# Kernel optimization log

Hardware: AMD Instinct MI355X
Metric: run time of the kernel (lower is better)

## Reference

```python
import jax, jax.numpy as jnp
import numpy as np

B, S, D = 2, 2048, 1024
H, HD = 16, 64
WIN = 256


def setup_inputs() -> dict:
    key = jax.random.key(0)
    ks = jax.random.split(key, 9)
    scale = 0.02
    x = jax.random.normal(ks[0], (B, S, D), dtype=jnp.float32)
    Wq = jax.random.normal(ks[1], (D, H * HD), dtype=jnp.float32) * scale
    Wk = jax.random.normal(ks[2], (D, H * HD), dtype=jnp.float32) * scale
    Wv = jax.random.normal(ks[3], (D, H * HD), dtype=jnp.float32) * scale
    Wo = jax.random.normal(ks[4], (H * HD, D), dtype=jnp.float32) * scale
    bq = jnp.zeros((H * HD,), jnp.float32)
    bk = jnp.zeros((H * HD,), jnp.float32)
    bv = jnp.zeros((H * HD,), jnp.float32)
    bo = jnp.zeros((D,), jnp.float32)
    return {"x": x, "Wq": Wq, "bq": bq, "Wk": Wk, "bk": bk,
            "Wv": Wv, "bv": bv, "Wo": Wo, "bo": bo}


def _band_mask(seq_len, window):
    # True where attention is DISALLOWED (matches torch masked positions).
    # mask=None in the original => prefix_size=0, row i attends to
    # j in [max(0, i - window), i]  (causal sliding window).
    i = jnp.arange(seq_len)[:, None]
    j = jnp.arange(seq_len)[None, :]
    return (j > i) | (j < i - window)


def reference(x, Wq, bq, Wk, bk, Wv, bv, Wo, bo):
    b, s, _ = x.shape
    q = (x @ Wq + bq).reshape(b, s, H, HD)
    k = (x @ Wk + bk).reshape(b, s, H, HD)
    v = (x @ Wv + bv).reshape(b, s, H, HD)
    scores = jnp.einsum("bihd,bjhd->bhij", q, k) / jnp.sqrt(jnp.float32(HD))
    mask = _band_mask(s, WIN)  # [s, s], broadcasts over batch, heads
    scores = jnp.where(mask[None, None, :, :], -jnp.inf, scores)
    attn = jax.nn.softmax(scores, axis=-1)  # dropout is identity at eval
    out = jnp.einsum("bhij,bjhd->bihd", attn, v).reshape(b, s, H * HD)
    return out @ Wo + bo
```

## Files before the change

kernel.cpp:

```cpp
#include <hip/hip_runtime.h>
#include <stdint.h>
#include <stddef.h>

#define S_LEN 2048
#define DMODEL 1024
#define NHEAD 16
#define HDIM 64
#define WINSZ 256
#define MROWS 4096
#define NQKV 3072

typedef __bf16 bf16x8 __attribute__((ext_vector_type(8)));
typedef float f32x4 __attribute__((ext_vector_type(4)));
typedef unsigned short us4 __attribute__((ext_vector_type(4)));
typedef unsigned short us8 __attribute__((ext_vector_type(8)));

#define MFMA16(a, b, c) __builtin_amdgcn_mfma_f32_16x16x32_bf16((a), (b), (c), 0, 0, 0)

__device__ __forceinline__ unsigned short f2b(float f) {
  union { float f; unsigned u; } v; v.f = f;
  unsigned u = v.u;
  unsigned r = (u + 0x7FFFu + ((u >> 16) & 1u)) >> 16;
  return (unsigned short)r;
}
__device__ __forceinline__ void storev(float* p, float v) { *p = v; }
__device__ __forceinline__ void storev(unsigned short* p, float v) { *p = f2b(v); }

__device__ __forceinline__ void gload_lds16(const unsigned short* g, unsigned short* l) {
  __builtin_amdgcn_global_load_lds(
      (const __attribute__((address_space(1))) unsigned int*)g,
      (__attribute__((address_space(3))) unsigned int*)l, 16, 0, 0);
}


__global__ void prep_kernel(const float* __restrict__ x,
                            const float* __restrict__ Wq, const float* __restrict__ Wk,
                            const float* __restrict__ Wv, const float* __restrict__ Wo,
                            const float* __restrict__ bq, const float* __restrict__ bk,
                            const float* __restrict__ bv,
                            unsigned short* __restrict__ xb, unsigned short* __restrict__ WqkvT,
                            unsigned short* __restrict__ WoT, float* __restrict__ bqkv) {
  __shared__ float tile[32][33];
  const int bid = blockIdx.x;
  const int tid = threadIdx.x;
  if (bid < 4096) {
    int i = (bid * 256 + tid) * 4;
    float4 v = *reinterpret_cast<const float4*>(x + i);
    us4 o;
    o[0] = f2b(v.x); o[1] = f2b(v.y); o[2] = f2b(v.z); o[3] = f2b(v.w);
    *reinterpret_cast<us4*>(xb + i) = o;
  } else if (bid < 8192) {
    int z = (bid - 4096) >> 10;
    int rem = (bid - 4096) & 1023;
    int bx = rem & 31, by = rem >> 5;
    const float* W = (z == 0) ? Wq : (z == 1) ? Wk : (z == 2) ? Wv : Wo;
    unsigned short* Wt = (z == 3) ? WoT : WqkvT + (size_t)z * DMODEL * DMODEL;
    int n0 = bx * 32, k0 = by * 32;
    int tx = tid & 31, ty = tid >> 5;
#pragma unroll
    for (int i = 0; i < 32; i += 8)
      tile[ty + i][tx] = W[(size_t)(k0 + ty + i) * DMODEL + n0 + tx];
    __syncthreads();
#pragma unroll
    for (int i = 0; i < 32; i += 8)
      Wt[(size_t)(n0 + ty + i) * DMODEL + k0 + tx] = f2b(tile[tx][ty + i]);
  } else {
    int i = (bid - 8192) * 256 + tid;
    if (i < DMODEL) {
      bqkv[i] = bq[i];
      bqkv[DMODEL + i] = bk[i];
      bqkv[2 * DMODEL + i] = bv[i];
    }
  }
}


__global__ __launch_bounds__(512, 4) void gemm8p_kernel(
    const unsigned short* __restrict__ A, const unsigned short* __restrict__ Bt,
    const float* __restrict__ bias, unsigned short* __restrict__ C, int N, int K) {
  __shared__ unsigned short As[2 * 128 * 64];
  __shared__ unsigned short Bs[2 * 192 * 64];
  const int tid = threadIdx.x;
  const int cpx = gridDim.x >> 3;
  const int nid = (blockIdx.x & 7) * cpx + (blockIdx.x >> 3);
  const int nbx = N / 192;
  const int by = nid / nbx, bx = nid - by * nbx;
  const int m0 = by * 128, n0 = bx * 192;
  const int wid = tid >> 6, l = tid & 63;
  const int wm = wid >> 2, wn = wid & 3;
  const int lr = l & 15, lg = l >> 4;
  const int srow = tid >> 3;
  const int scol = (tid & 7) * 8;
  const int scol_g = scol ^ (((tid >> 5) & 1) << 4);
  const int NT = K >> 6;

  f32x4 acc[4][3];
#pragma unroll
  for (int i = 0; i < 4; i++)
#pragma unroll
    for (int j = 0; j < 3; j++) acc[i][j] = (f32x4){0.f, 0.f, 0.f, 0.f};

  auto stage = [&](int buf, int kt) {
#pragma unroll
    for (int r = 0; r < 2; r++)
      gload_lds16(A + (size_t)(m0 + r * 64 + srow) * K + kt * 64 + scol_g,
                  &As[((buf * 2 + r) * 64 + srow) * 64 + scol]);
#pragma unroll
    for (int c = 0; c < 3; c++)
      gload_lds16(Bt + (size_t)(n0 + c * 64 + srow) * K + kt * 64 + scol_g,
                  &Bs[((buf * 3 + c) * 64 + srow) * 64 + scol]);
  };

  stage(0, 0);
  asm volatile("s_waitcnt vmcnt(0)" ::: "memory");
  __builtin_amdgcn_s_barrier();

  const int colr = (lg * 8) ^ (((lr >> 2) & 1) << 4);
  const int aB = (wm * 64 + lr) * 64 + colr;
  int bOff[3];
#pragma unroll
  for (int j = 0; j < 3; j++)
    bOff[j] = (wn * 48 + j * 16 + lr) * 64 + colr;

  int cur = 0;
#pragma unroll 1
  for (int t = 0; t < NT; t++) {
    if (t + 1 < NT) stage(cur ^ 1, t + 1);
    bf16x8 a[4][2], b[3][2];
#pragma unroll
    for (int i = 0; i < 4; i++)
#pragma unroll
      for (int kk = 0; kk < 2; kk++)
        a[i][kk] = *reinterpret_cast<const bf16x8*>(&As[cur * 8192 + i * 1024 + kk * 32 + aB]);
#pragma unroll
    for (int j = 0; j < 3; j++)
#pragma unroll
      for (int kk = 0; kk < 2; kk++)
        b[j][kk] = *reinterpret_cast<const bf16x8*>(&Bs[cur * 12288 + kk * 32 + bOff[j]]);
    __builtin_amdgcn_s_setprio(1);
#pragma unroll
    for (int i = 0; i < 4; i++)
#pragma unroll
      for (int j = 0; j < 3; j++)
#pragma unroll
        for (int kk = 0; kk < 2; kk++)
          acc[i][j] = MFMA16(a[i][kk], b[j][kk], acc[i][j]);
    __builtin_amdgcn_s_setprio(0);
    asm volatile("s_waitcnt vmcnt(0)" ::: "memory");
    __builtin_amdgcn_s_barrier();
    cur ^= 1;
  }

#pragma unroll
  for (int i = 0; i < 4; i++) {
    int row = m0 + wm * 64 + i * 16 + lg * 4;
#pragma unroll
    for (int j = 0; j < 3; j++) {
      int col = n0 + wn * 48 + j * 16 + lr;
      float bsv = bias[col];
#pragma unroll
      for (int r = 0; r < 4; r++)
        C[(size_t)(row + r) * N + col] = f2b(acc[i][j][r] + bsv);
    }
  }
}


template <typename OutT>
__global__ __launch_bounds__(256, 3) void gemm2p_kernel(
    const unsigned short* __restrict__ A, const unsigned short* __restrict__ Bt,
    const float* __restrict__ bias, OutT* __restrict__ C, int N, int K) {
  __shared__ unsigned short As[2 * 128 * 64];
  __shared__ unsigned short Bs[2 * 64 * 64];
  const int tid = threadIdx.x;
  const int cpx = gridDim.x >> 3;
  const int nid = (blockIdx.x & 7) * cpx + (blockIdx.x >> 3);
  const int nbx = N >> 6;
  const int by = nid / nbx, bx = nid - by * nbx;
  const int m0 = by * 128, n0 = bx * 64;
  const int w = tid >> 6, l = tid & 63;
  const int wm = (w >> 1) * 64, wn = (w & 1) * 32;
  const int lr = l & 15, lg = l >> 4;
  const int srow = tid >> 3;
  const int scol = (tid & 7) * 8;
  const int scol_g = scol ^ (((tid >> 5) & 1) << 4);
  const int NT = K >> 6;

  f32x4 acc[4][2];
#pragma unroll
  for (int i = 0; i < 4; i++)
#pragma unroll
    for (int j = 0; j < 2; j++) acc[i][j] = (f32x4){0.f, 0.f, 0.f, 0.f};

  auto stage = [&](int buf, int kt) {
#pragma unroll
    for (int r = 0; r < 4; r++)
      gload_lds16(A + (size_t)(m0 + r * 32 + srow) * K + kt * 64 + scol_g,
                  &As[(buf * 128 + r * 32 + srow) * 64 + scol]);
#pragma unroll
    for (int r = 0; r < 2; r++)
      gload_lds16(Bt + (size_t)(n0 + r * 32 + srow) * K + kt * 64 + scol_g,
                  &Bs[(buf * 64 + r * 32 + srow) * 64 + scol]);
  };

  stage(0, 0);
  asm volatile("s_waitcnt vmcnt(0)" ::: "memory");
  __builtin_amdgcn_s_barrier();

  const int colr = (lg * 8) ^ (((lr >> 2) & 1) << 4);
  const int aB = (wm + lr) * 64 + colr;
  const int bB = (wn + lr) * 64 + colr;

  int cur = 0;
#pragma unroll 1
  for (int t = 0; t < NT; t++) {
    if (t + 1 < NT) stage(cur ^ 1, t + 1);
    bf16x8 a[4][2], b[2][2];
#pragma unroll
    for (int i = 0; i < 4; i++)
#pragma unroll
      for (int kk = 0; kk < 2; kk++)
        a[i][kk] = *reinterpret_cast<const bf16x8*>(&As[cur * 8192 + i * 1024 + kk * 32 + aB]);
#pragma unroll
    for (int j = 0; j < 2; j++)
#pragma unroll
      for (int kk = 0; kk < 2; kk++)
        b[j][kk] = *reinterpret_cast<const bf16x8*>(&Bs[cur * 4096 + j * 1024 + kk * 32 + bB]);
    __builtin_amdgcn_s_setprio(1);
#pragma unroll
    for (int i = 0; i < 4; i++)
#pragma unroll
      for (int j = 0; j < 2; j++)
#pragma unroll
        for (int kk = 0; kk < 2; kk++)
          acc[i][j] = MFMA16(a[i][kk], b[j][kk], acc[i][j]);
    __builtin_amdgcn_s_setprio(0);
    asm volatile("s_waitcnt vmcnt(0)" ::: "memory");
    __builtin_amdgcn_s_barrier();
    cur ^= 1;
  }

#pragma unroll
  for (int i = 0; i < 4; i++) {
    int row = m0 + wm + i * 16 + lg * 4;
#pragma unroll
    for (int j = 0; j < 2; j++) {
      int col = n0 + wn + j * 16 + lr;
      float bsv = bias[col];
#pragma unroll
      for (int r = 0; r < 4; r++)
        storev(&C[(size_t)(row + r) * N + col], acc[i][j][r] + bsv);
    }
  }
}


__global__ __launch_bounds__(256) void attn_kernel(const unsigned short* __restrict__ qkv,
                                                   unsigned short* __restrict__ attnb) {
  __shared__ unsigned short Ks[64 * 72];
  __shared__ unsigned short Vt[64 * 72];
  __shared__ unsigned short Ps[4][16 * 72];

  const int tid = threadIdx.x;
  const int i0 = blockIdx.x * 64;
  const int h = blockIdx.y;
  const int b = blockIdx.z;
  const int w = tid >> 6, l = tid & 63;
  const int lr = l & 15, lg = l >> 4;
  const size_t rowb = (size_t)b * S_LEN;

  const unsigned short* qptr = qkv + (rowb + i0 + w * 16 + lr) * NQKV + h * HDIM;
  bf16x8 qa[2];
  qa[0] = *reinterpret_cast<const bf16x8*>(qptr + lg * 8);
  qa[1] = *reinterpret_cast<const bf16x8*>(qptr + 32 + lg * 8);

  f32x4 accO[4];
#pragma unroll
  for (int f = 0; f < 4; f++) accO[f] = (f32x4){0.f, 0.f, 0.f, 0.f};
  float Mv[4], Lv[4];
#pragma unroll
  for (int r = 0; r < 4; r++) { Mv[r] = -1e30f; Lv[r] = 0.f; }

  for (int c = 0; c < 5; c++) {
    int j0c = i0 - WINSZ + c * 64;
    if (j0c + 63 < 0) continue;
    __syncthreads();
    {
      int d8 = (tid & 7) * 8;
      int jl0 = tid >> 3;
#pragma unroll
      for (int it = 0; it < 2; it++) {
        int jl = jl0 + it * 32;
        int jg = j0c + jl;
        us8 kv = (us8){0, 0, 0, 0, 0, 0, 0, 0}, vv = (us8){0, 0, 0, 0, 0, 0, 0, 0};
        if (jg >= 0) {
          const unsigned short* kp = qkv + (rowb + jg) * NQKV + DMODEL + h * HDIM + d8;
          kv = *reinterpret_cast<const us8*>(kp);
          vv = *reinterpret_cast<const us8*>(kp + DMODEL);
        }
        *reinterpret_cast<us8*>(&Ks[jl * 72 + d8]) = kv;
#pragma unroll
        for (int e = 0; e < 8; e++) Vt[(d8 + e) * 72 + jl] = vv[e];
      }
    }
    __syncthreads();

    f32x4 sa[4];
#pragma unroll
    for (int f = 0; f < 4; f++) sa[f] = (f32x4){0.f, 0.f, 0.f, 0.f};
#pragma unroll
    for (int f = 0; f < 4; f++) {
      bf16x8 k0v = *reinterpret_cast<const bf16x8*>(&Ks[(f * 16 + lr) * 72 + lg * 8]);
      bf16x8 k1v = *reinterpret_cast<const bf16x8*>(&Ks[(f * 16 + lr) * 72 + 32 + lg * 8]);
      sa[f] = MFMA16(qa[0], k0v, sa[f]);
      sa[f] = MFMA16(qa[1], k1v, sa[f]);
    }
#pragma unroll
    for (int f = 0; f < 4; f++) {
      int jg = j0c + f * 16 + lr;
#pragma unroll
      for (int r = 0; r < 4; r++) {
        int irow = i0 + w * 16 + lg * 4 + r;
        float s = sa[f][r] * 0.125f;
        bool ok = (jg >= 0) && (jg <= irow) && (jg >= irow - WINSZ);
        sa[f][r] = ok ? s : -1e30f;
      }
    }
    float pm[4];
#pragma unroll
    for (int r = 0; r < 4; r++) {
      float m = fmaxf(fmaxf(sa[0][r], sa[1][r]), fmaxf(sa[2][r], sa[3][r]));
#pragma unroll
      for (int off = 1; off < 16; off <<= 1) m = fmaxf(m, __shfl_xor(m, off));
      pm[r] = m;
    }
#pragma unroll
    for (int r = 0; r < 4; r++) {
      float Mn = fmaxf(Mv[r], pm[r]);
      float sc = __expf(Mv[r] - Mn);
      Mv[r] = Mn;
      Lv[r] *= sc;
#pragma unroll
      for (int f = 0; f < 4; f++) accO[f][r] *= sc;
    }
    float rs[4] = {0.f, 0.f, 0.f, 0.f};
#pragma unroll
    for (int f = 0; f < 4; f++) {
#pragma unroll
      for (int r = 0; r < 4; r++) {
        float p = __expf(sa[f][r] - Mv[r]);
        rs[r] += p;
        Ps[w][(lg * 4 + r) * 72 + f * 16 + lr] = f2b(p);
      }
    }
#pragma unroll
    for (int r = 0; r < 4; r++) {
      float s = rs[r];
#pragma unroll
      for (int off = 1; off < 16; off <<= 1) s += __shfl_xor(s, off);
      Lv[r] += s;
    }
    bf16x8 pa0 = *reinterpret_cast<const bf16x8*>(&Ps[w][lr * 72 + lg * 8]);
    bf16x8 pa1 = *reinterpret_cast<const bf16x8*>(&Ps[w][lr * 72 + 32 + lg * 8]);
#pragma unroll
    for (int f = 0; f < 4; f++) {
      bf16x8 v0 = *reinterpret_cast<const bf16x8*>(&Vt[(f * 16 + lr) * 72 + lg * 8]);
      bf16x8 v1 = *reinterpret_cast<const bf16x8*>(&Vt[(f * 16 + lr) * 72 + 32 + lg * 8]);
      accO[f] = MFMA16(pa0, v0, accO[f]);
      accO[f] = MFMA16(pa1, v1, accO[f]);
    }
  }

#pragma unroll
  for (int f = 0; f < 4; f++) {
#pragma unroll
    for (int r = 0; r < 4; r++) {
      float o = accO[f][r] / Lv[r];
      int row = i0 + w * 16 + lg * 4 + r;
      attnb[(rowb + row) * DMODEL + h * HDIM + f * 16 + lr] = f2b(o);
    }
  }
}


extern "C" void kernel_launch(void* const* d_in, const int* in_sizes, int n_in,
                              void* d_out, int out_size, void* d_ws, size_t ws_size,
                              hipStream_t stream) {
  const float* x = (const float*)d_in[0];
  const float* Wq = (const float*)d_in[1];
  const float* bq = (const float*)d_in[2];
  const float* Wk = (const float*)d_in[3];
  const float* bk = (const float*)d_in[4];
  const float* Wv = (const float*)d_in[5];
  const float* bv = (const float*)d_in[6];
  const float* Wo = (const float*)d_in[7];
  const float* bo = (const float*)d_in[8];
  float* out = (float*)d_out;

  unsigned short* xb = (unsigned short*)d_ws;
  unsigned short* WqkvT = xb + (size_t)MROWS * DMODEL;
  unsigned short* WoT = WqkvT + (size_t)3 * DMODEL * DMODEL;
  unsigned short* QKV = WoT + (size_t)DMODEL * DMODEL;
  unsigned short* attnb = QKV + (size_t)MROWS * NQKV;
  float* bqkv = (float*)(attnb + (size_t)MROWS * DMODEL);

  prep_kernel<<<8196, 256, 0, stream>>>(x, Wq, Wk, Wv, Wo, bq, bk, bv,
                                        xb, WqkvT, WoT, bqkv);

  gemm8p_kernel<<<(NQKV / 192) * (MROWS / 128), 512, 0, stream>>>(
      xb, WqkvT, bqkv, QKV, NQKV, DMODEL);

  attn_kernel<<<dim3(S_LEN / 64, NHEAD, 2), 256, 0, stream>>>(QKV, attnb);

  gemm2p_kernel<float><<<(DMODEL / 64) * (MROWS / 128), 256, 0, stream>>>(
      attnb, WoT, bo, out, DMODEL, DMODEL);
}
```

Before: 90.23 us.

## Retile QKV GEMM to 256x128 single-buffer tiles and swizzle attention V transpose

Replaces the 128x192, 512-thread double-buffered QKV GEMM with a 256x128, 256-thread kernel that holds 8x4 accumulators per wave. It uses a single LDS buffer, loading the second k-half into registers before issuing the next stage's async loads. The change targets higher arithmetic intensity per LDS byte and fewer blocks, but reduces overlap and occupancy and raises register pressure. The attention kernel also XOR-swizzles the transposed V tile in LDS to cut bank conflicts on the scalar transpose stores.

```diff
diff --git a/kernel.cpp b/kernel.cpp
--- a/kernel.cpp
+++ b/kernel.cpp
@@ -75,88 +75,89 @@
 }
 
 
-__global__ __launch_bounds__(512, 4) void gemm8p_kernel(
+__global__ __launch_bounds__(256, 3) void gemmqkv_kernel(
     const unsigned short* __restrict__ A, const unsigned short* __restrict__ Bt,
     const float* __restrict__ bias, unsigned short* __restrict__ C, int N, int K) {
-  __shared__ unsigned short As[2 * 128 * 64];
-  __shared__ unsigned short Bs[2 * 192 * 64];
+  __shared__ unsigned short As[256 * 64];
+  __shared__ unsigned short Bs[128 * 64];
   const int tid = threadIdx.x;
   const int cpx = gridDim.x >> 3;
   const int nid = (blockIdx.x & 7) * cpx + (blockIdx.x >> 3);
-  const int nbx = N / 192;
+  const int nbx = N >> 7;
   const int by = nid / nbx, bx = nid - by * nbx;
-  const int m0 = by * 128, n0 = bx * 192;
-  const int wid = tid >> 6, l = tid & 63;
-  const int wm = wid >> 2, wn = wid & 3;
+  const int m0 = by * 256, n0 = bx * 128;
+  const int w = tid >> 6, l = tid & 63;
+  const int wm = w >> 1, wn = w & 1;
   const int lr = l & 15, lg = l >> 4;
   const int srow = tid >> 3;
   const int scol = (tid & 7) * 8;
   const int scol_g = scol ^ (((tid >> 5) & 1) << 4);
   const int NT = K >> 6;
 
-  f32x4 acc[4][3];
-#pragma unroll
-  for (int i = 0; i < 4; i++)
-#pragma unroll
-    for (int j = 0; j < 3; j++) acc[i][j] = (f32x4){0.f, 0.f, 0.f, 0.f};
-
-  auto stage = [&](int buf, int kt) {
-#pragma unroll
-    for (int r = 0; r < 2; r++)
-      gload_lds16(A + (size_t)(m0 + r * 64 + srow) * K + kt * 64 + scol_g,
-                  &As[((buf * 2 + r) * 64 + srow) * 64 + scol]);
-#pragma unroll
-    for (int c = 0; c < 3; c++)
-      gload_lds16(Bt + (size_t)(n0 + c * 64 + srow) * K + kt * 64 + scol_g,
-                  &Bs[((buf * 3 + c) * 64 + srow) * 64 + scol]);
+  f32x4 acc[8][4];
+#pragma unroll
+  for (int i = 0; i < 8; i++)
+#pragma unroll
+    for (int j = 0; j < 4; j++) acc[i][j] = (f32x4){0.f, 0.f, 0.f, 0.f};
+
+  auto stage = [&](int kt) {
+#pragma unroll
+    for (int r = 0; r < 8; r++)
+      gload_lds16(A + (size_t)(m0 + r * 32 + srow) * K + kt * 64 + scol_g,
+                  &As[(r * 32 + srow) * 64 + scol]);
+#pragma unroll
+    for (int r = 0; r < 4; r++)
+      gload_lds16(Bt + (size_t)(n0 + r * 32 + srow) * K + kt * 64 + scol_g,
+                  &Bs[(r * 32 + srow) * 64 + scol]);
   };
 
-  stage(0, 0);
-  asm volatile("s_waitcnt vmcnt(0)" ::: "memory");
-  __builtin_amdgcn_s_barrier();
+  stage(0);
 
   const int colr = (lg * 8) ^ (((lr >> 2) & 1) << 4);
-  const int aB = (wm * 64 + lr) * 64 + colr;
-  int bOff[3];
-#pragma unroll
-  for (int j = 0; j < 3; j++)
-    bOff[j] = (wn * 48 + j * 16 + lr) * 64 + colr;
-
-  int cur = 0;
+  const int aB = (wm * 128 + lr) * 64 + colr;
+  const int bB = (wn * 64 + lr) * 64 + colr;
+
 #pragma unroll 1
   for (int t = 0; t < NT; t++) {
-    if (t + 1 < NT) stage(cur ^ 1, t + 1);
-    bf16x8 a[4][2], b[3][2];
-#pragma unroll
-    for (int i = 0; i < 4; i++)
-#pragma unroll
-      for (int kk = 0; kk < 2; kk++)
-        a[i][kk] = *reinterpret_cast<const bf16x8*>(&As[cur * 8192 + i * 1024 + kk * 32 + aB]);
-#pragma unroll
-    for (int j = 0; j < 3; j++)
-#pragma unroll
-      for (int kk = 0; kk < 2; kk++)
-        b[j][kk] = *reinterpret_cast<const bf16x8*>(&Bs[cur * 12288 + kk * 32 + bOff[j]]);
+    __syncthreads();
+    bf16x8 a0[8], b0[4];
+#pragma unroll
+    for (int i = 0; i < 8; i++)
+      a0[i] = *reinterpret_cast<const bf16x8*>(&As[aB + i * 1024]);
+#pragma unroll
+    for (int j = 0; j < 4; j++)
+      b0[j] = *reinterpret_cast<const bf16x8*>(&Bs[bB + j * 1024]);
     __builtin_amdgcn_s_setprio(1);
 #pragma unroll
-    for (int i = 0; i < 4; i++)
-#pragma unroll
-      for (int j = 0; j < 3; j++)
-#pragma unroll
-        for (int kk = 0; kk < 2; kk++)
-          acc[i][j] = MFMA16(a[i][kk], b[j][kk], acc[i][j]);
+    for (int i = 0; i < 8; i++)
+#pragma unroll
+      for (int j = 0; j < 4; j++)
+        acc[i][j] = MFMA16(a0[i], b0[j], acc[i][j]);
     __builtin_amdgcn_s_setprio(0);
-    asm volatile("s_waitcnt vmcnt(0)" ::: "memory");
-    __builtin_amdgcn_s_barrier();
-    cur ^= 1;
-  }
-
-#pragma unroll
-  for (int i = 0; i < 4; i++) {
-    int row = m0 + wm * 64 + i * 16 + lg * 4;
-#pragma unroll
-    for (int j = 0; j < 3; j++) {
-      int col = n0 + wn * 48 + j * 16 + lr;
+    bf16x8 a1[8], b1[4];
+#pragma unroll
+    for (int i = 0; i < 8; i++)
+      a1[i] = *reinterpret_cast<const bf16x8*>(&As[aB + i * 1024 + 32]);
+#pragma unroll
+    for (int j = 0; j < 4; j++)
+      b1[j] = *reinterpret_cast<const bf16x8*>(&Bs[bB + j * 1024 + 32]);
+    __syncthreads();
+    if (t + 1 < NT) stage(t + 1);
+    __builtin_amdgcn_s_setprio(1);
+#pragma unroll
+    for (int i = 0; i < 8; i++)
+#pragma unroll
+      for (int j = 0; j < 4; j++)
+        acc[i][j] = MFMA16(a1[i], b1[j], acc[i][j]);
+    __builtin_amdgcn_s_setprio(0);
+  }
+
+#pragma unroll
+  for (int i = 0; i < 8; i++) {
+    int row = m0 + wm * 128 + i * 16 + lg * 4;
+#pragma unroll
+    for (int j = 0; j < 4; j++) {
+      int col = n0 + wn * 64 + j * 16 + lr;
       float bsv = bias[col];
 #pragma unroll
       for (int r = 0; r < 4; r++)
@@ -288,6 +289,7 @@
     {
       int d8 = (tid & 7) * 8;
       int jl0 = tid >> 3;
+      int swv = (tid & 3) << 3;
 #pragma unroll
       for (int it = 0; it < 2; it++) {
         int jl = jl0 + it * 32;
@@ -299,8 +301,9 @@
           vv = *reinterpret_cast<const us8*>(kp + DMODEL);
         }
         *reinterpret_cast<us8*>(&Ks[jl * 72 + d8]) = kv;
-#pragma unroll
-        for (int e = 0; e < 8; e++) Vt[(d8 + e) * 72 + jl] = vv[e];
+        int jsw = jl ^ swv;
+#pragma unroll
+        for (int e = 0; e < 8; e++) Vt[(d8 + e) * 72 + jsw] = vv[e];
       }
     }
     __syncthreads();
@@ -364,8 +367,9 @@
     bf16x8 pa1 = *reinterpret_cast<const bf16x8*>(&Ps[w][lr * 72 + 32 + lg * 8]);
 #pragma unroll
     for (int f = 0; f < 4; f++) {
-      bf16x8 v0 = *reinterpret_cast<const bf16x8*>(&Vt[(f * 16 + lr) * 72 + lg * 8]);
-      bf16x8 v1 = *reinterpret_cast<const bf16x8*>(&Vt[(f * 16 + lr) * 72 + 32 + lg * 8]);
+      int vsw = ((f * 2 + (lr >> 3)) & 3) << 3;
+      bf16x8 v0 = *reinterpret_cast<const bf16x8*>(&Vt[(f * 16 + lr) * 72 + ((lg * 8) ^ vsw)]);
+      bf16x8 v1 = *reinterpret_cast<const bf16x8*>(&Vt[(f * 16 + lr) * 72 + 32 + ((lg * 8) ^ vsw)]);
       accO[f] = MFMA16(pa0, v0, accO[f]);
       accO[f] = MFMA16(pa1, v1, accO[f]);
     }
@@ -407,7 +411,7 @@
   prep_kernel<<<8196, 256, 0, stream>>>(x, Wq, Wk, Wv, Wo, bq, bk, bv,
                                         xb, WqkvT, WoT, bqkv);
 
-  gemm8p_kernel<<<(NQKV / 192) * (MROWS / 128), 512, 0, stream>>>(
+  gemmqkv_kernel<<<(NQKV / 128) * (MROWS / 256), 256, 0, stream>>>(
       xb, WqkvT, bqkv, QKV, NQKV, DMODEL);
 
   attn_kernel<<<dim3(S_LEN / 64, NHEAD, 2), 256, 0, stream>>>(QKV, attnb);
```

Result: slower. 241.1 us (+167.2%).
